# Kernel optimization log

Measured on AMD Instinct MI355X. Metric: run time of the kernel, lower is better.

## Reference

```python
import jax, jax.numpy as jnp
import numpy as np
import math

N, S, D, H, L, F = 4, 2048, 512, 8, 4, 200
HD = D // H
EPS = 1e-5


def _pos_encoding(seq_len, d_model, dtype):
    pos = jnp.arange(seq_len, dtype=jnp.float32)[:, None]            # [S,1]
    div = jnp.exp(jnp.arange(0, d_model, 2, dtype=jnp.float32) * (-math.log(10000.0) / d_model))
    ang = pos * div                                                   # [S,D/2]
    pe = jnp.stack([jnp.sin(ang), jnp.cos(ang)], axis=-1).reshape(seq_len, d_model)
    return pe.astype(dtype)


def _layernorm(x, w, b):
    mu = jnp.mean(x, axis=-1, keepdims=True)
    var = jnp.mean(jnp.square(x - mu), axis=-1, keepdims=True)
    return (x - mu) * jax.lax.rsqrt(var + EPS) * w + b


def setup_inputs() -> dict:
    key = jax.random.key(0)
    ks = jax.random.split(key, 8)
    std = 0.02
    inp = {
        "features": jax.random.normal(ks[0], (N, S, D), dtype=jnp.float32),
        # attention projections, stored as [L, in, out] (math-equivalent to torch x @ W.T + b)
        "Wq": jax.random.normal(ks[1], (L, D, D), dtype=jnp.float32) * std,
        "bq": jnp.zeros((L, D), dtype=jnp.float32),
        "Wk": jax.random.normal(ks[2], (L, D, D), dtype=jnp.float32) * std,
        "bk": jnp.zeros((L, D), dtype=jnp.float32),
        "Wv": jax.random.normal(ks[3], (L, D, D), dtype=jnp.float32) * std,
        "bv": jnp.zeros((L, D), dtype=jnp.float32),
        "Wo": jax.random.normal(ks[4], (L, D, D), dtype=jnp.float32) * std,
        "bo": jnp.zeros((L, D), dtype=jnp.float32),
        # FFN
        "W1": jax.random.normal(ks[5], (L, D, F), dtype=jnp.float32) * std,
        "b1": jnp.zeros((L, F), dtype=jnp.float32),
        "W2": jax.random.normal(ks[6], (L, F, D), dtype=jnp.float32) * std,
        "b2": jnp.zeros((L, D), dtype=jnp.float32),
        # layernorms
        "ln1_w": jnp.ones((L, D), dtype=jnp.float32),
        "ln1_b": jnp.zeros((L, D), dtype=jnp.float32),
        "ln2_w": jnp.ones((L, D), dtype=jnp.float32),
        "ln2_b": jnp.zeros((L, D), dtype=jnp.float32),
    }
    return inp


def _encoder(features, Wq, bq, Wk, bk, Wv, bv, Wo, bo, W1, b1, W2, b2,
             ln1_w, ln1_b, ln2_w, ln2_b):
    n, s, d = features.shape
    x = features + _pos_encoding(s, d, features.dtype)[None]  # PositionalEncoding (dropout=identity in eval)
    scale = 1.0 / math.sqrt(HD)
    for l in range(L):
        # MultiHeadAttention: manual QK^T -> softmax -> AV
        q = (x @ Wq[l] + bq[l]).reshape(n, s, H, HD)
        k = (x @ Wk[l] + bk[l]).reshape(n, s, H, HD)
        v = (x @ Wv[l] + bv[l]).reshape(n, s, H, HD)
        attn = jnp.einsum("nshd,nthd->nhst", q, k) * scale          # [N,H,S,S]
        score = jax.nn.softmax(attn, axis=-1)
        y = jnp.einsum("nhst,nthd->nshd", score, v).reshape(n, s, d)
        attn_out = y @ Wo[l] + bo[l]
        x = _layernorm(x + attn_out, ln1_w[l], ln1_b[l])
        # FFN: linear2(relu(linear1(x)))
        ff = jax.nn.relu(x @ W1[l] + b1[l]) @ W2[l] + b2[l]
        x = _layernorm(x + ff, ln2_w[l], ln2_b[l])
    return x


def reference(features, Wq, bq, Wk, bk, Wv, bv, Wo, bo, W1, b1, W2, b2,
              ln1_w, ln1_b, ln2_w, ln2_b):
    return _encoder(features, Wq, bq, Wk, bk, Wv, bv, Wo, bo, W1, b1, W2, b2,
                    ln1_w, ln1_b, ln2_w, ln2_b)
```

## Files before the change

kernel.cpp:

```cpp
#include <hip/hip_runtime.h>
#include <hip/hip_bf16.h>
#include <cstdint>


typedef __bf16 bf16;
typedef __bf16 bf16x8 __attribute__((ext_vector_type(8)));
typedef __bf16 bf16x4 __attribute__((ext_vector_type(4)));
typedef short short4v __attribute__((ext_vector_type(4)));
typedef float f32x4 __attribute__((ext_vector_type(4)));

#define MFMA16(a, b, c) __builtin_amdgcn_mfma_f32_16x16x32_bf16((a), (b), (c), 0, 0, 0)

__device__ __forceinline__ f32x4 mfma_k16(bf16x4 a, bf16x4 b, f32x4 c) {
#if __has_builtin(__builtin_amdgcn_mfma_f32_16x16x16_bf16)
    return __builtin_amdgcn_mfma_f32_16x16x16_bf16(a, b, c, 0, 0, 0);
#else
    short4v as, bs;
    __builtin_memcpy(&as, &a, 8);
    __builtin_memcpy(&bs, &b, 8);
    return __builtin_amdgcn_mfma_f32_16x16x16bf16_1k(as, bs, c, 0, 0, 0);
#endif
}

static constexpr int NB   = 4;
static constexpr int SQ   = 2048;
static constexpr int DM   = 512;
static constexpr int NH   = 8;
static constexpr int HD   = 64;
static constexpr int NL   = 4;
static constexpr int FF   = 200;
static constexpr int FFP  = 256;
static constexpr int MTOK = NB * SQ;

__device__ __forceinline__ float fast_exp2(float x) {
#if __has_builtin(__builtin_amdgcn_exp2f)
    return __builtin_amdgcn_exp2f(x);
#else
    return exp2f(x);
#endif
}

__device__ __forceinline__ void gld16(bf16* l, const bf16* g) {
    __builtin_amdgcn_global_load_lds(
        (const __attribute__((address_space(1))) void*)g,
        (__attribute__((address_space(3))) void*)l, 16, 0, 0);
}

__global__ __launch_bounds__(256) void convw_kernel(
    const float* __restrict__ Wq, const float* __restrict__ Wk,
    const float* __restrict__ Wv, const float* __restrict__ Wo,
    const float* __restrict__ W1, const float* __restrict__ W2,
    bf16* __restrict__ wqkvt, bf16* __restrict__ wot,
    bf16* __restrict__ w1t, bf16* __restrict__ w2t)
{
    __shared__ float tile[32][33];
    const int z = blockIdx.z, l = z / 6, which = z % 6;
    const float* src; bf16* dst; int K, Nsrc, Npad, Kpad;
    switch (which) {
        case 0: src = Wq + (size_t)l*DM*DM; dst = wqkvt + (size_t)(l*3+0)*DM*DM; K=DM; Nsrc=DM; Npad=DM; Kpad=DM; break;
        case 1: src = Wk + (size_t)l*DM*DM; dst = wqkvt + (size_t)(l*3+1)*DM*DM; K=DM; Nsrc=DM; Npad=DM; Kpad=DM; break;
        case 2: src = Wv + (size_t)l*DM*DM; dst = wqkvt + (size_t)(l*3+2)*DM*DM; K=DM; Nsrc=DM; Npad=DM; Kpad=DM; break;
        case 3: src = Wo + (size_t)l*DM*DM; dst = wot   + (size_t)l*DM*DM;       K=DM; Nsrc=DM; Npad=DM; Kpad=DM; break;
        case 4: src = W1 + (size_t)l*DM*FF; dst = w1t   + (size_t)l*FFP*DM;      K=DM; Nsrc=FF; Npad=FFP; Kpad=DM; break;
        default:src = W2 + (size_t)l*FF*DM; dst = w2t   + (size_t)l*DM*FFP;      K=FF; Nsrc=DM; Npad=DM; Kpad=FFP; break;
    }
    const int k0 = blockIdx.x * 32, n0 = blockIdx.y * 32;
    if (k0 >= Kpad || n0 >= Npad) return;
    const int tr = threadIdx.x >> 3, tc = (threadIdx.x & 7) * 4;
    for (int c = 0; c < 4; c++) {
        int sr = k0 + tr, sc = n0 + tc + c;
        tile[tr][tc + c] = (sr < K && sc < Nsrc) ? src[(size_t)sr * Nsrc + sc] : 0.f;
    }
    __syncthreads();
    const int dr = n0 + tr;
    if (dr < Npad) {
        for (int c = 0; c < 4; c++) {
            int dc = k0 + tc + c;
            if (dc < Kpad) dst[(size_t)dr * Kpad + dc] = (bf16)tile[tc + c][tr];
        }
    }
}

__global__ __launch_bounds__(256) void posenc_kernel(
    const float* __restrict__ f, float* __restrict__ x, bf16* __restrict__ xb)
{
    const int t = blockIdx.x * 256 + threadIdx.x;
    const int d2 = t & 255, row = t >> 8, s = row & (SQ - 1);
    const float kfac = -0.03597789207803197f;
    float dv = __expf((float)d2 * kfac);
    float ang = (float)s * dv;
    float pe0 = sinf(ang), pe1 = cosf(ang);
    const size_t base = (size_t)row * DM + d2 * 2;
    float2 fv = *(const float2*)(f + base);
    float o0 = fv.x + pe0, o1 = fv.y + pe1;
    *(float2*)(x + base) = make_float2(o0, o1);
    union { bf16 h[2]; unsigned int u; } pk;
    pk.h[0] = (bf16)o0; pk.h[1] = (bf16)o1;
    *(unsigned int*)(xb + base) = pk.u;
}

__device__ __forceinline__ void gemm128_core(
    const bf16* __restrict__ A, const bf16* __restrict__ Wt, int K,
    int m0, int n0, bf16* As, bf16* Bs, f32x4 (&acc)[4][4])
{
    const int tid = threadIdx.x;
    const int w = tid >> 6, lane = tid & 63;
    const int l15 = lane & 15, quad = lane >> 4;
    const int srow = w * 16 + (lane >> 2);
    const int scol = (lane & 3) * 8;
    const bf16* Ag = A  + (size_t)(m0 + srow) * K + scol;
    const bf16* Bg = Wt + (size_t)(n0 + srow) * K + scol;
    bf16* AsW = As + w * 512;
    bf16* BsW = Bs + w * 512;
    const int wm = (w >> 1) * 64, wn = (w & 1) * 64;

    for (int k0 = 0; k0 < K; k0 += 32) {
        __syncthreads();
        gld16(AsW,        Ag + k0);
        gld16(AsW + 2048, Ag + (size_t)64 * K + k0);
        gld16(BsW,        Bg + k0);
        gld16(BsW + 2048, Bg + (size_t)64 * K + k0);
        asm volatile("s_waitcnt vmcnt(0)" ::: "memory");
        __syncthreads();

        bf16x8 af[4], bfr[4];
        #pragma unroll
        for (int i = 0; i < 4; i++)
            af[i] = *(const bf16x8*)&As[(wm + i * 16 + l15) * 32 + quad * 8];
        #pragma unroll
        for (int j = 0; j < 4; j++)
            bfr[j] = *(const bf16x8*)&Bs[(wn + j * 16 + l15) * 32 + quad * 8];
        #pragma unroll
        for (int i = 0; i < 4; i++)
            #pragma unroll
            for (int j = 0; j < 4; j++)
                acc[i][j] = MFMA16(af[i], bfr[j], acc[i][j]);
    }
}

__global__ __launch_bounds__(256, 3) void gemm64_kernel(
    const bf16* __restrict__ A, const bf16* __restrict__ Wt,
    const float* __restrict__ bias, int nbias,
    float* __restrict__ outf, bf16* __restrict__ outb,
    int K, int Nc, int mode)
{
    __shared__ alignas(16) bf16 As[128 * 32];
    __shared__ alignas(16) bf16 Bs[64 * 32];
    const int m0 = blockIdx.x * 128, n0 = blockIdx.y * 64;
    const int tid = threadIdx.x;
    const int w = tid >> 6, lane = tid & 63;
    const int l15 = lane & 15, quad = lane >> 4;
    const int srow = w * 16 + (lane >> 2);
    const int scol = (lane & 3) * 8;
    const bf16* Ag = A  + (size_t)(m0 + srow) * K + scol;
    const bf16* Bg = Wt + (size_t)(n0 + srow) * K + scol;
    bf16* AsW = As + w * 512;
    bf16* BsW = Bs + w * 512;
    const int wm = (w >> 1) * 64, wn = (w & 1) * 32;
    f32x4 acc[4][2] = {};

    for (int k0 = 0; k0 < K; k0 += 32) {
        __syncthreads();
        gld16(AsW,        Ag + k0);
        gld16(AsW + 2048, Ag + (size_t)64 * K + k0);
        gld16(BsW,        Bg + k0);
        asm volatile("s_waitcnt vmcnt(0)" ::: "memory");
        __syncthreads();

        bf16x8 af[4], bfr[2];
        #pragma unroll
        for (int i = 0; i < 4; i++)
            af[i] = *(const bf16x8*)&As[(wm + i * 16 + l15) * 32 + quad * 8];
        #pragma unroll
        for (int j = 0; j < 2; j++)
            bfr[j] = *(const bf16x8*)&Bs[(wn + j * 16 + l15) * 32 + quad * 8];
        #pragma unroll
        for (int i = 0; i < 4; i++)
            #pragma unroll
            for (int j = 0; j < 2; j++)
                acc[i][j] = MFMA16(af[i], bfr[j], acc[i][j]);
    }

    #pragma unroll
    for (int j = 0; j < 2; j++) {
        const int col = n0 + wn + j * 16 + l15;
        const float bv = (col < nbias) ? bias[col] : 0.f;
        #pragma unroll
        for (int i = 0; i < 4; i++) {
            const int rbase = m0 + wm + i * 16 + quad * 4;
            #pragma unroll
            for (int r = 0; r < 4; r++) {
                float v = acc[i][j][r] + bv;
                const int row = rbase + r;
                const size_t idx = (size_t)row * Nc + col;
                if (mode == 0)      outf[idx] = v;
                else if (mode == 1) outb[idx] = (bf16)v;
                else                outb[idx] = (bf16)fmaxf(v, 0.f);
            }
        }
    }
}

__global__ __launch_bounds__(256, 3) void gemm128_qkv_kernel(
    const bf16* __restrict__ xb, const bf16* __restrict__ Wt,
    const float* __restrict__ bq, const float* __restrict__ bk,
    const float* __restrict__ bv,
    bf16* __restrict__ qb, bf16* __restrict__ kb, bf16* __restrict__ vtb)
{
    __shared__ alignas(16) bf16 As[128 * 32];
    __shared__ alignas(16) bf16 Bs[128 * 32];
    const int m0 = blockIdx.x * 128, n0 = blockIdx.y * 128;
    f32x4 acc[4][4] = {};
    gemm128_core(xb, Wt, DM, m0, n0, As, Bs, acc);

    const int lane = threadIdx.x & 63;
    const int l15 = lane & 15, quad = lane >> 4;
    const int w = threadIdx.x >> 6;
    const int wm = (w >> 1) * 64, wn = (w & 1) * 64;
    const int which = n0 >> 9;
    const float* bias = (which == 0) ? bq : (which == 1) ? bk : bv;
    const float scale = (which == 0) ? 0.18033688f : 1.f;
    #pragma unroll
    for (int j = 0; j < 4; j++) {
        const int c = (n0 & 511) + wn + j * 16 + l15;
        const float bvv = bias[c];
        #pragma unroll
        for (int i = 0; i < 4; i++) {
            const int rbase = m0 + wm + i * 16 + quad * 4;
            #pragma unroll
            for (int r = 0; r < 4; r++) {
                float v = (acc[i][j][r] + bvv) * scale;
                const int row = rbase + r;
                if (which == 0)      qb[(size_t)row * DM + c] = (bf16)v;
                else if (which == 1) kb[(size_t)row * DM + c] = (bf16)v;
                else {
                    const int n = row >> 11, s = row & (SQ - 1);
                    const int h = c >> 6, hd = c & 63;
                    vtb[((size_t)(((n << 3) | h) << 6 | hd) << 11) | s] = (bf16)v;
                }
            }
        }
    }
}

__global__ __launch_bounds__(256, 2) void attn_kernel(
    const bf16* __restrict__ qb, const bf16* __restrict__ kb,
    const bf16* __restrict__ vtb,
    bf16* __restrict__ opart0, bf16* __restrict__ opart1,
    float* __restrict__ lpart)
{
    __shared__ alignas(16) bf16 Kt[2][64][72];
    __shared__ alignas(16) bf16 Vt[2 * 64 * 68];
    const int tid = threadIdx.x;
    const int w = tid >> 6, lane = tid & 63;
    const int l15 = lane & 15, quad = lane >> 4;
    const int id = blockIdx.x;
    const int kvhalf = id & 1;
    const int nh = (id >> 1) & 31;
    const int qblk = id >> 6;
    const int n = nh >> 3, h = nh & 7;
    const int q0 = qblk * 256 + w * 64;
    const int kvbase = kvhalf * (SQ / 2);
    const bf16* qbase = qb + (size_t)n * SQ * DM + h * HD;
    const bf16* kbase = kb + (size_t)n * SQ * DM + h * HD;
    const bf16* vbase = vtb + (size_t)nh * HD * SQ;

    bf16x8 qf[4][2];
    #pragma unroll
    for (int mi = 0; mi < 4; mi++)
        #pragma unroll
        for (int hh = 0; hh < 2; hh++)
            qf[mi][hh] = *(const bf16x8*)(qbase + (size_t)(q0 + mi*16 + l15) * DM + hh*32 + quad*8);

    f32x4 o[4][4] = {};
    float lsum[4] = {0.f, 0.f, 0.f, 0.f};

    const int srow = tid >> 2, seg = (tid & 3) * 16;
    const bf16* krow = kbase + (size_t)(kvbase + srow) * DM + seg;
    const bf16* vrow = vbase + (size_t)srow * SQ + kvbase + seg;

    auto storeV = [&](int buf, bf16x8 a, bf16x8 b) {
        bf16* d = &Vt[(buf * 64 + srow) * 68 + seg];
        bf16x4 p0, p1, p2, p3;
        #pragma unroll
        for (int i = 0; i < 4; i++) { p0[i]=a[i]; p1[i]=a[i+4]; p2[i]=b[i]; p3[i]=b[i+4]; }
        *(bf16x4*)(d)      = p0;
        *(bf16x4*)(d + 4)  = p1;
        *(bf16x4*)(d + 8)  = p2;
        *(bf16x4*)(d + 12) = p3;
    };

    {
        bf16x8 k0 = *(const bf16x8*)(krow);
        bf16x8 k1 = *(const bf16x8*)(krow + 8);
        bf16x8 v0 = *(const bf16x8*)(vrow);
        bf16x8 v1 = *(const bf16x8*)(vrow + 8);
        *(bf16x8*)&Kt[0][srow][seg]     = k0;
        *(bf16x8*)&Kt[0][srow][seg + 8] = k1;
        storeV(0, v0, v1);
    }

    const int NT = SQ / 128;
    for (int jt = 0; jt < NT; jt++) {
        const int buf = jt & 1;
        __syncthreads();
        const bool pre = (jt + 1 < NT);
        bf16x8 k0, k1, v0, v1;
        if (pre) {
            const bf16* kp = krow + (size_t)(jt + 1) * 64 * DM;
            const bf16* vp = vrow + (jt + 1) * 64;
            k0 = *(const bf16x8*)(kp);
            k1 = *(const bf16x8*)(kp + 8);
            v0 = *(const bf16x8*)(vp);
            v1 = *(const bf16x8*)(vp + 8);
        }

        #pragma unroll
        for (int s4 = 0; s4 < 4; s4++) {
            bf16x8 kf0 = *(const bf16x8*)&Kt[buf][s4*16 + l15][quad*8];
            bf16x8 kf1 = *(const bf16x8*)&Kt[buf][s4*16 + l15][32 + quad*8];
            bf16x4 pf[4];
            #pragma unroll
            for (int mi = 0; mi < 4; mi++) {
                f32x4 sacc = {};
                sacc = MFMA16(kf0, qf[mi][0], sacc);
                sacc = MFMA16(kf1, qf[mi][1], sacc);
                float p0 = fast_exp2(sacc[0]);
                float p1 = fast_exp2(sacc[1]);
                float p2 = fast_exp2(sacc[2]);
                float p3 = fast_exp2(sacc[3]);
                lsum[mi] += (p0 + p1) + (p2 + p3);
                bf16x4 pk;
                pk[0] = (bf16)p0; pk[1] = (bf16)p1;
                pk[2] = (bf16)p2; pk[3] = (bf16)p3;
                pf[mi] = pk;
            }
            #pragma unroll
            for (int d4 = 0; d4 < 4; d4++) {
                bf16x4 vf = *(const bf16x4*)&Vt[(buf*64 + d4*16 + l15) * 68 + s4*16 + quad*4];
                #pragma unroll
                for (int mi = 0; mi < 4; mi++)
                    o[mi][d4] = mfma_k16(pf[mi], vf, o[mi][d4]);
            }
        }

        if (pre) {
            *(bf16x8*)&Kt[buf^1][srow][seg]     = k0;
            *(bf16x8*)&Kt[buf^1][srow][seg + 8] = k1;
            storeV(buf^1, v0, v1);
        }
    }

    #pragma unroll
    for (int mi = 0; mi < 4; mi++) {
        lsum[mi] += __shfl_xor(lsum[mi], 16, 64);
        lsum[mi] += __shfl_xor(lsum[mi], 32, 64);
    }
    if (lane < 16) {
        const int qg = (nh << 11) + q0 + lane;
        #pragma unroll
        for (int mi = 0; mi < 4; mi++)
            lpart[(kvhalf << 16) + qg + mi * 16] = lsum[mi];
    }

    bf16* op = kvhalf ? opart1 : opart0;
    #pragma unroll
    for (int mi = 0; mi < 4; mi++) {
        #pragma unroll
        for (int d4 = 0; d4 < 4; d4++) {
            const int col = h * HD + d4 * 16 + l15;
            #pragma unroll
            for (int r = 0; r < 4; r++) {
                const int row = n * SQ + q0 + mi*16 + quad*4 + r;
                op[(size_t)row * DM + col] = (bf16)o[mi][d4][r];
            }
        }
    }
}

__global__ __launch_bounds__(256) void attn_combine_kernel(
    const bf16* o0, const bf16* o1, const float* __restrict__ lpart,
    bf16* yb)
{
    const int w = threadIdx.x >> 6, lane = threadIdx.x & 63;
    const size_t row = (size_t)blockIdx.x * 4 + w;
    const int q = (int)(row & (SQ - 1));
    const int nh = (int)(row >> 11) * 8 + (lane >> 3);
    const float rl = 1.f / (lpart[(nh << 11) + q] + lpart[(1 << 16) + (nh << 11) + q]);
    const size_t base = row * DM + lane * 8;
    bf16x8 a = *(const bf16x8*)(o0 + base);
    bf16x8 b = *(const bf16x8*)(o1 + base);
    bf16x8 y;
    #pragma unroll
    for (int i = 0; i < 8; i++)
        y[i] = (bf16)(((float)a[i] + (float)b[i]) * rl);
    *(bf16x8*)(yb + base) = y;
}

__global__ __launch_bounds__(256) void ln_kernel(
    const float* __restrict__ res, const float* __restrict__ add,
    const float* __restrict__ g, const float* __restrict__ beta,
    float* __restrict__ outf, bf16* __restrict__ outb)
{
    const int w = threadIdx.x >> 6, lane = threadIdx.x & 63;
    const size_t row = (size_t)blockIdx.x * 4 + w;
    const float4* rp = (const float4*)(res + row * DM);
    const float4* ap = (const float4*)(add + row * DM);
    float4 v[2];
    float s = 0.f, s2 = 0.f;
    #pragma unroll
    for (int i = 0; i < 2; i++) {
        const int idx = i * 64 + lane;
        float4 a = rp[idx], c = ap[idx];
        float x0 = a.x + c.x, x1 = a.y + c.y, x2 = a.z + c.z, x3 = a.w + c.w;
        v[i] = make_float4(x0, x1, x2, x3);
        s  += x0 + x1 + x2 + x3;
        s2 += x0*x0 + x1*x1 + x2*x2 + x3*x3;
    }
    for (int m = 1; m < 64; m <<= 1) {
        s  += __shfl_xor(s,  m, 64);
        s2 += __shfl_xor(s2, m, 64);
    }
    const float mean = s * (1.f / DM);
    const float var  = s2 * (1.f / DM) - mean * mean;
    const float rstd = rsqrtf(var + 1e-5f);
    #pragma unroll
    for (int i = 0; i < 2; i++) {
        const int idx = i * 64 + lane;
        float4 gw = ((const float4*)g)[idx], bw = ((const float4*)beta)[idx];
        float o0 = (v[i].x - mean) * rstd * gw.x + bw.x;
        float o1 = (v[i].y - mean) * rstd * gw.y + bw.y;
        float o2 = (v[i].z - mean) * rstd * gw.z + bw.z;
        float o3 = (v[i].w - mean) * rstd * gw.w + bw.w;
        ((float4*)(outf + row * DM))[idx] = make_float4(o0, o1, o2, o3);
        union { bf16 h[4]; uint2 u; } pk;
        pk.h[0] = (bf16)o0; pk.h[1] = (bf16)o1; pk.h[2] = (bf16)o2; pk.h[3] = (bf16)o3;
        *(uint2*)(outb + row * DM + idx * 4) = pk.u;
    }
}

extern "C" void kernel_launch(void* const* d_in, const int* in_sizes, int n_in,
                              void* d_out, int out_size, void* d_ws, size_t ws_size,
                              hipStream_t stream)
{
    const float* features = (const float*)d_in[0];
    const float* Wq  = (const float*)d_in[1];
    const float* bq  = (const float*)d_in[2];
    const float* Wk  = (const float*)d_in[3];
    const float* bk  = (const float*)d_in[4];
    const float* Wv  = (const float*)d_in[5];
    const float* bv  = (const float*)d_in[6];
    const float* Wo  = (const float*)d_in[7];
    const float* bo  = (const float*)d_in[8];
    const float* W1  = (const float*)d_in[9];
    const float* b1  = (const float*)d_in[10];
    const float* W2  = (const float*)d_in[11];
    const float* b2  = (const float*)d_in[12];
    const float* ln1w = (const float*)d_in[13];
    const float* ln1b = (const float*)d_in[14];
    const float* ln2w = (const float*)d_in[15];
    const float* ln2b = (const float*)d_in[16];
    float* outp = (float*)d_out;

    char* p = (char*)d_ws;
    size_t off = 0;
    auto alloc = [&](size_t bytes) { void* r = p + off; off = (off + bytes + 255) & ~(size_t)255; return r; };
    const size_t tokD = (size_t)MTOK * DM;
    float* x     = (float*)alloc(tokD * 4);
    float* tmp   = (float*)alloc(tokD * 4);
    bf16* xb     = (bf16*)alloc(tokD * 2);
    bf16* qb     = (bf16*)alloc(tokD * 2);
    bf16* kb     = (bf16*)alloc(tokD * 2);
    bf16* vtb    = (bf16*)alloc(tokD * 2);
    bf16* yb     = (bf16*)alloc(tokD * 2);
    bf16* opart1 = (bf16*)alloc(tokD * 2);
    float* lpart = (float*)alloc(2 * 65536 * 4);
    bf16* ffh    = (bf16*)alloc((size_t)MTOK * FFP * 2);
    bf16* wqkvt  = (bf16*)alloc((size_t)NL * 3 * DM * DM * 2);
    bf16* wot    = (bf16*)alloc((size_t)NL * DM * DM * 2);
    bf16* w1t    = (bf16*)alloc((size_t)NL * FFP * DM * 2);
    bf16* w2t    = (bf16*)alloc((size_t)NL * DM * FFP * 2);
    (void)ws_size; (void)in_sizes; (void)n_in; (void)out_size;

    convw_kernel<<<dim3(16, 16, NL * 6), 256, 0, stream>>>(
        Wq, Wk, Wv, Wo, W1, W2, wqkvt, wot, w1t, w2t);

    posenc_kernel<<<MTOK, 256, 0, stream>>>(features, x, xb);

    for (int l = 0; l < NL; l++) {
        const bf16* wqkvt_l = wqkvt + (size_t)l * 3 * DM * DM;
        gemm128_qkv_kernel<<<dim3(MTOK / 128, 1536 / 128), 256, 0, stream>>>(
            xb, wqkvt_l, bq + l*DM, bk + l*DM, bv + l*DM, qb, kb, vtb);
        attn_kernel<<<512, 256, 0, stream>>>(qb, kb, vtb, yb, opart1, lpart);
        attn_combine_kernel<<<MTOK / 4, 256, 0, stream>>>(yb, opart1, lpart, yb);
        gemm64_kernel<<<dim3(MTOK / 128, DM / 64), 256, 0, stream>>>(
            yb, wot + (size_t)l*DM*DM, bo + l*DM, DM, tmp, nullptr, DM, DM, 0);
        ln_kernel<<<MTOK / 4, 256, 0, stream>>>(x, tmp, ln1w + l*DM, ln1b + l*DM, x, xb);
        gemm64_kernel<<<dim3(MTOK / 128, FFP / 64), 256, 0, stream>>>(
            xb, w1t + (size_t)l*FFP*DM, b1 + l*FF, FF, nullptr, ffh, DM, FFP, 2);
        gemm64_kernel<<<dim3(MTOK / 128, DM / 64), 256, 0, stream>>>(
            ffh, w2t + (size_t)l*DM*FFP, b2 + l*DM, DM, tmp, nullptr, FFP, DM, 0);
        float* outdst = (l == NL - 1) ? outp : x;
        ln_kernel<<<MTOK / 4, 256, 0, stream>>>(x, tmp, ln2w + l*DM, ln2b + l*DM, outdst, xb);
    }
}
```

Before: 642.4 us.

## Fuse attention split-KV combine into Wo GEMM and use K32 MFMA for PV

Removes the separate attn_combine kernel by having the Wo projection GEMM read both partial attention outputs, add them, and scale them by the reciprocal softmax denominators while staging its A tile. The attention kernel now processes 32 keys per step so the PV product uses the 16x16x32 MFMA instead of the K16 variant, and it computes the row sums with an MFMA against a ones vector rather than scalar adds and shuffles. This saves one kernel launch and a full read/write pass over the attention output, at the cost of the GEMM reading two A operands plus per-head scales, and of row sums built from bf16-rounded probabilities.

```diff
diff --git a/kernel.cpp b/kernel.cpp
--- a/kernel.cpp
+++ b/kernel.cpp
@@ -6,21 +6,9 @@
 typedef __bf16 bf16;
 typedef __bf16 bf16x8 __attribute__((ext_vector_type(8)));
 typedef __bf16 bf16x4 __attribute__((ext_vector_type(4)));
-typedef short short4v __attribute__((ext_vector_type(4)));
 typedef float f32x4 __attribute__((ext_vector_type(4)));
 
 #define MFMA16(a, b, c) __builtin_amdgcn_mfma_f32_16x16x32_bf16((a), (b), (c), 0, 0, 0)
-
-__device__ __forceinline__ f32x4 mfma_k16(bf16x4 a, bf16x4 b, f32x4 c) {
-#if __has_builtin(__builtin_amdgcn_mfma_f32_16x16x16_bf16)
-    return __builtin_amdgcn_mfma_f32_16x16x16_bf16(a, b, c, 0, 0, 0);
-#else
-    short4v as, bs;
-    __builtin_memcpy(&as, &a, 8);
-    __builtin_memcpy(&bs, &b, 8);
-    return __builtin_amdgcn_mfma_f32_16x16x16bf16_1k(as, bs, c, 0, 0, 0);
-#endif
-}
 
 static constexpr int NB   = 4;
 static constexpr int SQ   = 2048;
@@ -197,6 +185,93 @@
                 else if (mode == 1) outb[idx] = (bf16)v;
                 else                outb[idx] = (bf16)fmaxf(v, 0.f);
             }
+        }
+    }
+}
+
+__global__ __launch_bounds__(256, 3) void gemm_wo_kernel(
+    const bf16* __restrict__ o0, const bf16* __restrict__ o1,
+    const float* __restrict__ lpart,
+    const bf16* __restrict__ Wt, const float* __restrict__ bias,
+    float* __restrict__ outf)
+{
+    __shared__ alignas(16) bf16 As[128 * 32];
+    __shared__ alignas(16) bf16 Bs[64 * 32];
+    const int m0 = blockIdx.x * 128, n0 = blockIdx.y * 64;
+    const int tid = threadIdx.x;
+    const int w = tid >> 6, lane = tid & 63;
+    const int l15 = lane & 15, quad = lane >> 4;
+    const int srow = w * 16 + (lane >> 2);
+    const int scol = (lane & 3) * 8;
+    const int row0 = m0 + srow, row1 = row0 + 64;
+    const bf16* Bg = Wt + (size_t)(n0 + srow) * DM + scol;
+    bf16* BsW = Bs + w * 512;
+    bf16* AsD0 = As + w * 512 + lane * 8;
+    bf16* AsD1 = AsD0 + 2048;
+    const int wm = (w >> 1) * 64, wn = (w & 1) * 32;
+
+    const int b0 = (((row0 >> 11) * 8) << 11) | (row0 & (SQ - 1));
+    const int b1 = (((row1 >> 11) * 8) << 11) | (row1 & (SQ - 1));
+    float rl0[8], rl1[8];
+    #pragma unroll
+    for (int h = 0; h < 8; h++) {
+        rl0[h] = 1.f / (lpart[b0 + (h << 11)] + lpart[65536 + b0 + (h << 11)]);
+        rl1[h] = 1.f / (lpart[b1 + (h << 11)] + lpart[65536 + b1 + (h << 11)]);
+    }
+
+    const bf16* A0g  = o0 + (size_t)row0 * DM + scol;
+    const bf16* A0g2 = o0 + (size_t)row1 * DM + scol;
+    const bf16* A1g  = o1 + (size_t)row0 * DM + scol;
+    const bf16* A1g2 = o1 + (size_t)row1 * DM + scol;
+    f32x4 acc[4][2] = {};
+
+    #pragma unroll
+    for (int h = 0; h < 8; h++) {
+        #pragma unroll
+        for (int kk = 0; kk < 2; kk++) {
+            const int k0 = h * 64 + kk * 32;
+            __syncthreads();
+            bf16x8 a0 = *(const bf16x8*)(A0g  + k0);
+            bf16x8 c0 = *(const bf16x8*)(A1g  + k0);
+            bf16x8 a1 = *(const bf16x8*)(A0g2 + k0);
+            bf16x8 c1 = *(const bf16x8*)(A1g2 + k0);
+            gld16(BsW, Bg + k0);
+            bf16x8 s0, s1;
+            #pragma unroll
+            for (int i = 0; i < 8; i++) {
+                s0[i] = (bf16)(((float)a0[i] + (float)c0[i]) * rl0[h]);
+                s1[i] = (bf16)(((float)a1[i] + (float)c1[i]) * rl1[h]);
+            }
+            *(bf16x8*)AsD0 = s0;
+            *(bf16x8*)AsD1 = s1;
+            asm volatile("s_waitcnt vmcnt(0)" ::: "memory");
+            __syncthreads();
+
+            bf16x8 af[4], bfr[2];
+            #pragma unroll
+            for (int i = 0; i < 4; i++)
+                af[i] = *(const bf16x8*)&As[(wm + i * 16 + l15) * 32 + quad * 8];
+            #pragma unroll
+            for (int j = 0; j < 2; j++)
+                bfr[j] = *(const bf16x8*)&Bs[(wn + j * 16 + l15) * 32 + quad * 8];
+            #pragma unroll
+            for (int i = 0; i < 4; i++)
+                #pragma unroll
+                for (int j = 0; j < 2; j++)
+                    acc[i][j] = MFMA16(af[i], bfr[j], acc[i][j]);
+        }
+    }
+
+    #pragma unroll
+    for (int j = 0; j < 2; j++) {
+        const int col = n0 + wn + j * 16 + l15;
+        const float bv = bias[col];
+        #pragma unroll
+        for (int i = 0; i < 4; i++) {
+            const int rbase = m0 + wm + i * 16 + quad * 4;
+            #pragma unroll
+            for (int r = 0; r < 4; r++)
+                outf[(size_t)(rbase + r) * DM + col] = acc[i][j][r] + bv;
         }
     }
 }
@@ -272,8 +347,12 @@
         for (int hh = 0; hh < 2; hh++)
             qf[mi][hh] = *(const bf16x8*)(qbase + (size_t)(q0 + mi*16 + l15) * DM + hh*32 + quad*8);
 
+    bf16x8 ones8;
+    #pragma unroll
+    for (int i = 0; i < 8; i++) ones8[i] = (bf16)1.0f;
+
     f32x4 o[4][4] = {};
-    float lsum[4] = {0.f, 0.f, 0.f, 0.f};
+    f32x4 lacc[4] = {};
 
     const int srow = tid >> 2, seg = (tid & 3) * 16;
     const bf16* krow = kbase + (size_t)(kvbase + srow) * DM + seg;
@@ -316,31 +395,39 @@
         }
 
         #pragma unroll
-        for (int s4 = 0; s4 < 4; s4++) {
-            bf16x8 kf0 = *(const bf16x8*)&Kt[buf][s4*16 + l15][quad*8];
-            bf16x8 kf1 = *(const bf16x8*)&Kt[buf][s4*16 + l15][32 + quad*8];
-            bf16x4 pf[4];
+        for (int sp = 0; sp < 2; sp++) {
+            bf16x8 kfA0 = *(const bf16x8*)&Kt[buf][sp*32 + l15][quad*8];
+            bf16x8 kfA1 = *(const bf16x8*)&Kt[buf][sp*32 + l15][32 + quad*8];
+            bf16x8 kfB0 = *(const bf16x8*)&Kt[buf][sp*32 + 16 + l15][quad*8];
+            bf16x8 kfB1 = *(const bf16x8*)&Kt[buf][sp*32 + 16 + l15][32 + quad*8];
+            bf16x8 pf[4];
             #pragma unroll
             for (int mi = 0; mi < 4; mi++) {
-                f32x4 sacc = {};
-                sacc = MFMA16(kf0, qf[mi][0], sacc);
-                sacc = MFMA16(kf1, qf[mi][1], sacc);
-                float p0 = fast_exp2(sacc[0]);
-                float p1 = fast_exp2(sacc[1]);
-                float p2 = fast_exp2(sacc[2]);
-                float p3 = fast_exp2(sacc[3]);
-                lsum[mi] += (p0 + p1) + (p2 + p3);
-                bf16x4 pk;
-                pk[0] = (bf16)p0; pk[1] = (bf16)p1;
-                pk[2] = (bf16)p2; pk[3] = (bf16)p3;
-                pf[mi] = pk;
+                f32x4 sa = {}, sb = {};
+                sa = MFMA16(kfA0, qf[mi][0], sa);
+                sa = MFMA16(kfA1, qf[mi][1], sa);
+                sb = MFMA16(kfB0, qf[mi][0], sb);
+                sb = MFMA16(kfB1, qf[mi][1], sb);
+                bf16x8 p;
+                #pragma unroll
+                for (int r = 0; r < 4; r++) {
+                    p[r]     = (bf16)fast_exp2(sa[r]);
+                    p[r + 4] = (bf16)fast_exp2(sb[r]);
+                }
+                pf[mi] = p;
+                lacc[mi] = MFMA16(p, ones8, lacc[mi]);
             }
             #pragma unroll
             for (int d4 = 0; d4 < 4; d4++) {
-                bf16x4 vf = *(const bf16x4*)&Vt[(buf*64 + d4*16 + l15) * 68 + s4*16 + quad*4];
+                const bf16* vp2 = &Vt[(buf*64 + d4*16 + l15) * 68 + sp*32 + quad*4];
+                bf16x4 vlo = *(const bf16x4*)(vp2);
+                bf16x4 vhi = *(const bf16x4*)(vp2 + 16);
+                bf16x8 vf;
+                #pragma unroll
+                for (int i = 0; i < 4; i++) { vf[i] = vlo[i]; vf[i+4] = vhi[i]; }
                 #pragma unroll
                 for (int mi = 0; mi < 4; mi++)
-                    o[mi][d4] = mfma_k16(pf[mi], vf, o[mi][d4]);
+                    o[mi][d4] = MFMA16(pf[mi], vf, o[mi][d4]);
             }
         }
 
@@ -351,16 +438,13 @@
         }
     }
 
-    #pragma unroll
-    for (int mi = 0; mi < 4; mi++) {
-        lsum[mi] += __shfl_xor(lsum[mi], 16, 64);
-        lsum[mi] += __shfl_xor(lsum[mi], 32, 64);
-    }
-    if (lane < 16) {
-        const int qg = (nh << 11) + q0 + lane;
-        #pragma unroll
-        for (int mi = 0; mi < 4; mi++)
-            lpart[(kvhalf << 16) + qg + mi * 16] = lsum[mi];
+    if (l15 == 0) {
+        const int base = (kvhalf << 16) + (nh << 11) + q0 + quad * 4;
+        #pragma unroll
+        for (int mi = 0; mi < 4; mi++) {
+            float4 v4 = make_float4(lacc[mi][0], lacc[mi][1], lacc[mi][2], lacc[mi][3]);
+            *(float4*)&lpart[base + mi * 16] = v4;
+        }
     }
 
     bf16* op = kvhalf ? opart1 : opart0;
@@ -376,25 +460,6 @@
             }
         }
     }
-}
-
-__global__ __launch_bounds__(256) void attn_combine_kernel(
-    const bf16* o0, const bf16* o1, const float* __restrict__ lpart,
-    bf16* yb)
-{
-    const int w = threadIdx.x >> 6, lane = threadIdx.x & 63;
-    const size_t row = (size_t)blockIdx.x * 4 + w;
-    const int q = (int)(row & (SQ - 1));
-    const int nh = (int)(row >> 11) * 8 + (lane >> 3);
-    const float rl = 1.f / (lpart[(nh << 11) + q] + lpart[(1 << 16) + (nh << 11) + q]);
-    const size_t base = row * DM + lane * 8;
-    bf16x8 a = *(const bf16x8*)(o0 + base);
-    bf16x8 b = *(const bf16x8*)(o1 + base);
-    bf16x8 y;
-    #pragma unroll
-    for (int i = 0; i < 8; i++)
-        y[i] = (bf16)(((float)a[i] + (float)b[i]) * rl);
-    *(bf16x8*)(yb + base) = y;
 }
 
 __global__ __launch_bounds__(256) void ln_kernel(
@@ -472,7 +537,7 @@
     bf16* qb     = (bf16*)alloc(tokD * 2);
     bf16* kb     = (bf16*)alloc(tokD * 2);
     bf16* vtb    = (bf16*)alloc(tokD * 2);
-    bf16* yb     = (bf16*)alloc(tokD * 2);
+    bf16* opart0 = (bf16*)alloc(tokD * 2);
     bf16* opart1 = (bf16*)alloc(tokD * 2);
     float* lpart = (float*)alloc(2 * 65536 * 4);
     bf16* ffh    = (bf16*)alloc((size_t)MTOK * FFP * 2);
@@ -491,10 +556,9 @@
         const bf16* wqkvt_l = wqkvt + (size_t)l * 3 * DM * DM;
         gemm128_qkv_kernel<<<dim3(MTOK / 128, 1536 / 128), 256, 0, stream>>>(
             xb, wqkvt_l, bq + l*DM, bk + l*DM, bv + l*DM, qb, kb, vtb);
-        attn_kernel<<<512, 256, 0, stream>>>(qb, kb, vtb, yb, opart1, lpart);
-        attn_combine_kernel<<<MTOK / 4, 256, 0, stream>>>(yb, opart1, lpart, yb);
-        gemm64_kernel<<<dim3(MTOK / 128, DM / 64), 256, 0, stream>>>(
-            yb, wot + (size_t)l*DM*DM, bo + l*DM, DM, tmp, nullptr, DM, DM, 0);
+        attn_kernel<<<512, 256, 0, stream>>>(qb, kb, vtb, opart0, opart1, lpart);
+        gemm_wo_kernel<<<dim3(MTOK / 128, DM / 64), 256, 0, stream>>>(
+            opart0, opart1, lpart, wot + (size_t)l*DM*DM, bo + l*DM, tmp);
         ln_kernel<<<MTOK / 4, 256, 0, stream>>>(x, tmp, ln1w + l*DM, ln1b + l*DM, x, xb);
         gemm64_kernel<<<dim3(MTOK / 128, FFP / 64), 256, 0, stream>>>(
             xb, w1t + (size_t)l*FFP*DM, b1 + l*FF, FF, nullptr, ffh, DM, FFP, 2);
```

Result: faster. 627.9 us (-2.3%).
